# Optimization experiments

Hardware: AMD Instinct MI355X
Metric: run time of the kernel (lower is better)

## Reference

```python
import jax, jax.numpy as jnp
import numpy as np

B, S, D_IN, H = 4, 2048, 1024, 1024


def setup_inputs() -> dict:
    key = jax.random.key(0)
    k1, k2, k3 = jax.random.split(key, 3)
    qkv = jax.random.normal(k1, (B, S, D_IN), dtype=jnp.float32)
    # True = position is masked out (torch masked_fill semantics)
    attention_mask = jax.random.randint(k2, (B, S), 0, 2).astype(jnp.bool_)
    W_qkv = jax.random.normal(k3, (D_IN, 3 * H), dtype=jnp.float32) * (1.0 / np.sqrt(D_IN))
    b_qkv = jnp.zeros((3 * H,), dtype=jnp.float32)
    return {"qkv": qkv, "attention_mask": attention_mask, "W_qkv": W_qkv, "b_qkv": b_qkv}


def reference(qkv, attention_mask, W_qkv, b_qkv):
    # fused QKV projection: (B, S, 3H)
    proj = jnp.einsum("bsd,dh->bsh", qkv, W_qkv) + b_qkv
    q, k, v = jnp.split(proj, 3, axis=-1)  # each (B, S, H)
    scaling_factor = jnp.asarray(H, dtype=q.dtype) ** 0.5
    q = q * scaling_factor  # NOTE: original multiplies (not divides) by sqrt(H)
    scores = jnp.einsum("bqh,bkh->bqk", q, k)  # (B, S, S)
    # mask broadcasts over the query dim: masked keys get -inf
    neg_inf = jnp.asarray(-jnp.inf, dtype=scores.dtype)
    scores = jnp.where(attention_mask[:, None, :], neg_inf, scores)
    distributions = jax.nn.softmax(scores, axis=-1)  # dropout p=0.0 -> identity
    return jnp.einsum("bqk,bkh->bqh", distributions, v)
```

## Files before the change

kernel.cpp:

```cpp
#include <hip/hip_runtime.h>
#include <stdint.h>


#define S_LEN 2048
#define BATCH 4
#define DIN   1024
#define HDIM  1024
#define N3H   3072
#define NTOK  8192

typedef unsigned short u16;
typedef __attribute__((ext_vector_type(8))) short bf16x8;
typedef __attribute__((ext_vector_type(4))) float f32x4;
typedef __attribute__((ext_vector_type(16))) float f32x16;
typedef __attribute__((ext_vector_type(4))) unsigned short u16x4;

__device__ __forceinline__ u16 f2bf(float x) {
  union { float f; unsigned u; } c; c.f = x;
  unsigned r = c.u + 0x7fffu + ((c.u >> 16) & 1u);
  return (u16)(r >> 16);
}
__device__ __forceinline__ float bf2f(u16 h) {
  union { unsigned u; float f; } c; c.u = ((unsigned)h) << 16;
  return c.f;
}

__device__ __forceinline__ void gload16(const void* g, void* lds) {
  auto* gp = reinterpret_cast<const __attribute__((address_space(1))) void*>(
      reinterpret_cast<uintptr_t>(g));
  auto* lp = reinterpret_cast<__attribute__((address_space(3))) void*>(
      (unsigned)reinterpret_cast<uintptr_t>(lds));
  __builtin_amdgcn_global_load_lds(gp, lp, 16, 0, 0);
}

__device__ __forceinline__ void stage_tile(const u16* __restrict__ g, int ld,
                                           u16* lds, int wave, int lane) {
  const int rlane = lane >> 3;
  const int kb    = (lane & 7) ^ (rlane & 7);
#pragma unroll
  for (int h = 0; h < 4; ++h) {
    const int instr = wave * 4 + h;
    const u16* gp = g + (size_t)(instr * 8 + rlane) * ld + kb * 8;
    gload16(gp, (char*)lds + instr * 1024);
  }
}

__device__ __forceinline__ void stage_tile_idx(
    const u16* __restrict__ gbase, const int* __restrict__ idxb, int jbase,
    int k0, u16* lds, int wave, int lane) {
  const int rlane = lane >> 3;
  const int kb    = (lane & 7) ^ (rlane & 7);
#pragma unroll
  for (int h = 0; h < 4; ++h) {
    const int instr = wave * 4 + h;
    const int s = idxb[jbase + instr * 8 + rlane];
    const u16* gp = gbase + (size_t)s * DIN + k0 + kb * 8;
    gload16(gp, (char*)lds + instr * 1024);
  }
}

__device__ __forceinline__ bf16x8 frag32(const u16* t, int wq, int sub, int kh,
                                         int lane) {
  const int r5   = lane & 31;
  const int row  = wq * 64 + sub * 32 + r5;
  const int slot = (kh * 2 + (lane >> 5)) ^ (r5 & 7);
  return *(const bf16x8*)(t + row * 64 + slot * 8);
}

__device__ __forceinline__ void gemm_core_split(
    const u16* __restrict__ Ah, const u16* __restrict__ Al,
    const u16* __restrict__ Bh, const u16* __restrict__ Bl,
    int lda, int ldb, int K, f32x16 acc[2][2])
{
  __shared__ __align__(16) u16 lds[4 * 8192];
  u16* aH = lds;           u16* aL = lds + 8192;
  u16* bH = lds + 16384;   u16* bL = lds + 24576;
  const int tid  = threadIdx.x;
  const int wave = tid >> 6, lane = tid & 63;
  const int wm = wave >> 1, wn = wave & 1;

#pragma unroll
  for (int i = 0; i < 2; ++i)
#pragma unroll
    for (int j = 0; j < 2; ++j)
#pragma unroll
      for (int r = 0; r < 16; ++r) acc[i][j][r] = 0.f;

  for (int k0 = 0; k0 < K; k0 += 64) {
    stage_tile(Ah + k0, lda, aH, wave, lane);
    stage_tile(Al + k0, lda, aL, wave, lane);
    stage_tile(Bh + k0, ldb, bH, wave, lane);
    stage_tile(Bl + k0, ldb, bL, wave, lane);
    __syncthreads();

#pragma unroll
    for (int kh = 0; kh < 4; ++kh) {
      bf16x8 fah[2], fal[2];
#pragma unroll
      for (int i = 0; i < 2; ++i) {
        fah[i] = frag32(aH, wm, i, kh, lane);
        fal[i] = frag32(aL, wm, i, kh, lane);
      }
#pragma unroll
      for (int j = 0; j < 2; ++j) {
        const bf16x8 fbh = frag32(bH, wn, j, kh, lane);
        const bf16x8 fbl = frag32(bL, wn, j, kh, lane);
#pragma unroll
        for (int i = 0; i < 2; ++i) {
          acc[i][j] = __builtin_amdgcn_mfma_f32_32x32x16_bf16(fah[i], fbh, acc[i][j], 0, 0, 0);
          acc[i][j] = __builtin_amdgcn_mfma_f32_32x32x16_bf16(fah[i], fbl, acc[i][j], 0, 0, 0);
          acc[i][j] = __builtin_amdgcn_mfma_f32_32x32x16_bf16(fal[i], fbh, acc[i][j], 0, 0, 0);
        }
      }
    }
    __syncthreads();
  }
}

__device__ __forceinline__ void gemm_core_split_idx(
    const u16* __restrict__ Ah, const u16* __restrict__ Al,
    const int* __restrict__ idxb, int jbase,
    const u16* __restrict__ Bh, const u16* __restrict__ Bl,
    f32x16 acc[2][2])
{
  __shared__ __align__(16) u16 lds[4 * 8192];
  u16* aH = lds;           u16* aL = lds + 8192;
  u16* bH = lds + 16384;   u16* bL = lds + 24576;
  const int tid  = threadIdx.x;
  const int wave = tid >> 6, lane = tid & 63;
  const int wm = wave >> 1, wn = wave & 1;

#pragma unroll
  for (int i = 0; i < 2; ++i)
#pragma unroll
    for (int j = 0; j < 2; ++j)
#pragma unroll
      for (int r = 0; r < 16; ++r) acc[i][j][r] = 0.f;

  for (int k0 = 0; k0 < DIN; k0 += 64) {
    stage_tile_idx(Ah, idxb, jbase, k0, aH, wave, lane);
    stage_tile_idx(Al, idxb, jbase, k0, aL, wave, lane);
    stage_tile(Bh + k0, DIN, bH, wave, lane);
    stage_tile(Bl + k0, DIN, bL, wave, lane);
    __syncthreads();

#pragma unroll
    for (int kh = 0; kh < 4; ++kh) {
      bf16x8 fah[2], fal[2];
#pragma unroll
      for (int i = 0; i < 2; ++i) {
        fah[i] = frag32(aH, wm, i, kh, lane);
        fal[i] = frag32(aL, wm, i, kh, lane);
      }
#pragma unroll
      for (int j = 0; j < 2; ++j) {
        const bf16x8 fbh = frag32(bH, wn, j, kh, lane);
        const bf16x8 fbl = frag32(bL, wn, j, kh, lane);
#pragma unroll
        for (int i = 0; i < 2; ++i) {
          acc[i][j] = __builtin_amdgcn_mfma_f32_32x32x16_bf16(fah[i], fbh, acc[i][j], 0, 0, 0);
          acc[i][j] = __builtin_amdgcn_mfma_f32_32x32x16_bf16(fah[i], fbl, acc[i][j], 0, 0, 0);
          acc[i][j] = __builtin_amdgcn_mfma_f32_32x32x16_bf16(fal[i], fbh, acc[i][j], 0, 0, 0);
        }
      }
    }
    __syncthreads();
  }
}

__device__ __forceinline__ void gemm_core_plain(
    const u16* __restrict__ A, const u16* __restrict__ B,
    int lda, int ldb, int K, f32x16 acc[2][2])
{
  __shared__ __align__(16) u16 lds[2 * 8192];
  u16* aT = lds; u16* bT = lds + 8192;
  const int tid  = threadIdx.x;
  const int wave = tid >> 6, lane = tid & 63;
  const int wm = wave >> 1, wn = wave & 1;

#pragma unroll
  for (int i = 0; i < 2; ++i)
#pragma unroll
    for (int j = 0; j < 2; ++j)
#pragma unroll
      for (int r = 0; r < 16; ++r) acc[i][j][r] = 0.f;

  for (int k0 = 0; k0 < K; k0 += 64) {
    stage_tile(A + k0, lda, aT, wave, lane);
    stage_tile(B + k0, ldb, bT, wave, lane);
    __syncthreads();
#pragma unroll
    for (int kh = 0; kh < 4; ++kh) {
      bf16x8 fa[2];
#pragma unroll
      for (int i = 0; i < 2; ++i) fa[i] = frag32(aT, wm, i, kh, lane);
#pragma unroll
      for (int j = 0; j < 2; ++j) {
        const bf16x8 fb = frag32(bT, wn, j, kh, lane);
#pragma unroll
        for (int i = 0; i < 2; ++i)
          acc[i][j] = __builtin_amdgcn_mfma_f32_32x32x16_bf16(fa[i], fb, acc[i][j], 0, 0, 0);
      }
    }
    __syncthreads();
  }
}

__device__ __forceinline__ void gemm_core_plain_idx(
    const u16* __restrict__ A, const int* __restrict__ idxb, int jbase,
    const u16* __restrict__ B, f32x16 acc[2][2])
{
  __shared__ __align__(16) u16 lds[2 * 8192];
  u16* aT = lds; u16* bT = lds + 8192;
  const int tid  = threadIdx.x;
  const int wave = tid >> 6, lane = tid & 63;
  const int wm = wave >> 1, wn = wave & 1;

#pragma unroll
  for (int i = 0; i < 2; ++i)
#pragma unroll
    for (int j = 0; j < 2; ++j)
#pragma unroll
      for (int r = 0; r < 16; ++r) acc[i][j][r] = 0.f;

  for (int k0 = 0; k0 < DIN; k0 += 64) {
    stage_tile_idx(A, idxb, jbase, k0, aT, wave, lane);
    stage_tile(B + k0, DIN, bT, wave, lane);
    __syncthreads();
#pragma unroll
    for (int kh = 0; kh < 4; ++kh) {
      bf16x8 fa[2];
#pragma unroll
      for (int i = 0; i < 2; ++i) fa[i] = frag32(aT, wm, i, kh, lane);
#pragma unroll
      for (int j = 0; j < 2; ++j) {
        const bf16x8 fb = frag32(bT, wn, j, kh, lane);
#pragma unroll
        for (int i = 0; i < 2; ++i)
          acc[i][j] = __builtin_amdgcn_mfma_f32_32x32x16_bf16(fa[i], fb, acc[i][j], 0, 0, 0);
      }
    }
    __syncthreads();
  }
}

#define ROW32(r, lane) (((r) & 3) + 8 * ((r) >> 2) + 4 * ((lane) >> 5))

__global__ void prep_kernel(const unsigned char* __restrict__ m,
                            int* __restrict__ idx, int* __restrict__ kcount) {
  __shared__ int isBool;
  if (threadIdx.x == 0) isBool = 0;
  __syncthreads();
  for (int i = threadIdx.x; i < NTOK; i += 256)
    if ((i & 3) && m[i]) isBool = 1;
  __syncthreads();
  const int stride = isBool ? 1 : 4;
  const int wave = threadIdx.x >> 6, lane = threadIdx.x & 63;
  const int b = wave;
  const int base = b * S_LEN;
  int running = 0;
#pragma unroll 1
  for (int c = 0; c < S_LEN / 64; ++c) {
    const int s = c * 64 + lane;
    const int um = (m[(size_t)(base + s) * stride] == 0);
    const unsigned long long bal = __ballot(um);
    const int pre = (int)__popcll(bal & ((1ULL << lane) - 1ULL));
    if (um) idx[base + running + pre] = s;
    running += (int)__popcll(bal);
  }
  if (lane == 0) kcount[b] = running;
  for (int j = running + lane; j < S_LEN; j += 64) idx[base + j] = 0;
}

__global__ __launch_bounds__(256) void split_f32_kernel(
    const float* __restrict__ x, u16* __restrict__ hi, u16* __restrict__ lo) {
  const int i = (blockIdx.x * 256 + threadIdx.x) * 4;
  const f32x4 v = *(const f32x4*)(x + i);
  u16x4 h, l;
#pragma unroll
  for (int c = 0; c < 4; ++c) {
    h[c] = f2bf(v[c]);
    l[c] = f2bf(v[c] - bf2f(h[c]));
  }
  *(u16x4*)(hi + i) = h;
  *(u16x4*)(lo + i) = l;
}

__global__ __launch_bounds__(256) void splitWT_kernel(
    const float* __restrict__ W, u16* __restrict__ whi, u16* __restrict__ wlo) {
  __shared__ float tile[32][33];
  const int t = threadIdx.x;
  const int n0 = blockIdx.x * 32;
  const int d0 = blockIdx.y * 32;
  const int dr = t >> 3, nc = (t & 7) * 4;
  const f32x4 v = *(const f32x4*)(W + (size_t)(d0 + dr) * N3H + n0 + nc);
#pragma unroll
  for (int c = 0; c < 4; ++c) tile[dr][nc + c] = v[c];
  __syncthreads();
  const int nr = t >> 3, dc = (t & 7) * 4;
  u16x4 h, l;
#pragma unroll
  for (int c = 0; c < 4; ++c) {
    const float x = tile[dc + c][nr];
    h[c] = f2bf(x);
    l[c] = f2bf(x - bf2f(h[c]));
  }
  const size_t o = (size_t)(n0 + nr) * DIN + d0 + dc;
  *(u16x4*)(whi + o) = h;
  *(u16x4*)(wlo + o) = l;
}

__global__ __launch_bounds__(256, 2) void proj_q_kernel(
    const u16* __restrict__ Ahi, const u16* __restrict__ Alo,
    const u16* __restrict__ Whi, const u16* __restrict__ Wlo,
    const float* __restrict__ bias,
    u16* __restrict__ qhi, u16* __restrict__ qlo)
{
  const int bx = blockIdx.x, by = blockIdx.y;
  f32x16 acc[2][2];
  gemm_core_split(Ahi + (size_t)by * 128 * DIN, Alo + (size_t)by * 128 * DIN,
                  Whi + (size_t)bx * 128 * DIN, Wlo + (size_t)bx * 128 * DIN,
                  DIN, DIN, DIN, acc);
  const int lane = threadIdx.x & 63, wave = threadIdx.x >> 6;
  const int wm = wave >> 1, wn = wave & 1;
#pragma unroll
  for (int i = 0; i < 2; ++i) {
#pragma unroll
    for (int j = 0; j < 2; ++j) {
#pragma unroll
      for (int r = 0; r < 16; ++r) {
        const int row = by * 128 + wm * 64 + i * 32 + ROW32(r, lane);
        const int col = bx * 128 + wn * 64 + j * 32 + (lane & 31);
        const float v = acc[i][j][r] + bias[col];
        const u16 h = f2bf(v);
        const u16 l = f2bf(v - bf2f(h));
        const size_t idx = (size_t)row * HDIM + col;
        qhi[idx] = h; qlo[idx] = l;
      }
    }
  }
}

__global__ __launch_bounds__(256, 2) void proj_k_kernel(
    const u16* __restrict__ Ahi, const u16* __restrict__ Alo,
    const u16* __restrict__ Whi, const u16* __restrict__ Wlo,
    const float* __restrict__ bias,
    const int* __restrict__ idx, const int* __restrict__ kcount,
    u16* __restrict__ khi, u16* __restrict__ klo)
{
  const int id = blockIdx.x;
  const int t  = id >> 5;
  const int rs = id & 31;
  const int b  = rs >> 3;
  const int bx = rs & 7;
  const int cnt = kcount[b];
  if (t * 128 >= cnt) return;

  f32x16 acc[2][2];
  gemm_core_split_idx(Ahi + (size_t)b * S_LEN * DIN, Alo + (size_t)b * S_LEN * DIN,
                      idx + b * S_LEN, t * 128,
                      Whi + (size_t)(HDIM + bx * 128) * DIN,
                      Wlo + (size_t)(HDIM + bx * 128) * DIN, acc);
  const int lane = threadIdx.x & 63, wave = threadIdx.x >> 6;
  const int wm = wave >> 1, wn = wave & 1;
#pragma unroll
  for (int i = 0; i < 2; ++i) {
#pragma unroll
    for (int j = 0; j < 2; ++j) {
#pragma unroll
      for (int r = 0; r < 16; ++r) {
        const int jl   = t * 128 + wm * 64 + i * 32 + ROW32(r, lane);
        const int hcol = bx * 128 + wn * 64 + j * 32 + (lane & 31);
        const float v = acc[i][j][r] + bias[HDIM + hcol];
        const u16 h = f2bf(v);
        const u16 l = f2bf(v - bf2f(h));
        const size_t o = ((size_t)b * S_LEN + jl) * HDIM + hcol;
        khi[o] = h; klo[o] = l;
      }
    }
  }
}

__global__ __launch_bounds__(256, 2) void proj_v_kernel(
    const u16* __restrict__ Ahi, const u16* __restrict__ Whi,
    const float* __restrict__ bias,
    const int* __restrict__ idx, const int* __restrict__ kcount,
    u16* __restrict__ vt)
{
  const int id = blockIdx.x;
  const int t  = id >> 5;
  const int rs = id & 31;
  const int b  = rs >> 3;
  const int bx = rs & 7;
  const int cnt = kcount[b];
  if (t * 128 >= cnt) return;

  f32x16 acc[2][2];
  gemm_core_plain_idx(Ahi + (size_t)b * S_LEN * DIN, idx + b * S_LEN, t * 128,
                      Whi + (size_t)(2048 + bx * 128) * DIN, acc);
  const int lane = threadIdx.x & 63, wave = threadIdx.x >> 6;
  const int wm = wave >> 1, wn = wave & 1;
#pragma unroll
  for (int i = 0; i < 2; ++i) {
#pragma unroll
    for (int j = 0; j < 2; ++j) {
#pragma unroll
      for (int r = 0; r < 16; ++r) {
        const int jl   = t * 128 + wm * 64 + i * 32 + ROW32(r, lane);
        const int hcol = bx * 128 + wn * 64 + j * 32 + (lane & 31);
        const float v = acc[i][j][r] + bias[2 * HDIM + hcol];
        vt[((size_t)b * HDIM + hcol) * S_LEN + jl] = f2bf(v);
      }
    }
  }
}

__global__ __launch_bounds__(256, 2) void scores_kernel(
    const u16* __restrict__ qhi, const u16* __restrict__ qlo,
    const u16* __restrict__ khi, const u16* __restrict__ klo,
    const int* __restrict__ kcount, float* __restrict__ scores)
{
  const int id = blockIdx.x;
  const int bx = id >> 6;
  const int b  = (id >> 4) & 3;
  const int by = id & 15;
  const int cnt = kcount[b];
  if (bx * 128 >= cnt) return;

  f32x16 acc[2][2];
  const size_t qoff = ((size_t)b * S_LEN + by * 128) * HDIM;
  const size_t koff = ((size_t)b * S_LEN + bx * 128) * HDIM;
  gemm_core_split(qhi + qoff, qlo + qoff, khi + koff, klo + koff,
                  HDIM, HDIM, HDIM, acc);
  const int lane = threadIdx.x & 63, wave = threadIdx.x >> 6;
  const int wm = wave >> 1, wn = wave & 1;
#pragma unroll
  for (int i = 0; i < 2; ++i) {
#pragma unroll
    for (int j = 0; j < 2; ++j) {
#pragma unroll
      for (int rr = 0; rr < 16; ++rr) {
        const int q   = by * 128 + wm * 64 + i * 32 + ROW32(rr, lane);
        const int key = bx * 128 + wn * 64 + j * 32 + (lane & 31);
        scores[((size_t)b * S_LEN + q) * S_LEN + key] = 32.0f * acc[i][j][rr];
      }
    }
  }
}

__global__ __launch_bounds__(256) void softmax_kernel(
    float* __restrict__ scores, const int* __restrict__ kcount) {
  const int wave = threadIdx.x >> 6, lane = threadIdx.x & 63;
  const int row = blockIdx.x * 4 + wave;
  const int b = row >> 11;
  const int cnt = kcount[b];
  const int nc = (cnt + 255) >> 8;
  float* srow = scores + (size_t)row * S_LEN;
  const float ninf = -__builtin_inff();

  f32x4 v[8];
  float m = ninf;
#pragma unroll
  for (int c = 0; c < 8; ++c) {
    if (c < nc) {
      v[c] = ((const f32x4*)srow)[c * 64 + lane];
      const int j0 = c * 256 + lane * 4;
#pragma unroll
      for (int e = 0; e < 4; ++e) {
        if (j0 + e >= cnt) v[c][e] = ninf;
        m = fmaxf(m, v[c][e]);
      }
    }
  }
#pragma unroll
  for (int o = 32; o > 0; o >>= 1) m = fmaxf(m, __shfl_xor(m, o));

  float s = 0.f;
#pragma unroll
  for (int c = 0; c < 8; ++c) {
    if (c < nc) {
#pragma unroll
      for (int e = 0; e < 4; ++e) {
        v[c][e] = __expf(v[c][e] - m);
        s += v[c][e];
      }
    }
  }
#pragma unroll
  for (int o = 32; o > 0; o >>= 1) s += __shfl_xor(s, o);
  const float inv = 1.0f / s;

  u16* prow = (u16*)srow;
#pragma unroll
  for (int c = 0; c < 8; ++c) {
    if (c < nc) {
      u16x4 o4 = { f2bf(v[c][0] * inv), f2bf(v[c][1] * inv),
                   f2bf(v[c][2] * inv), f2bf(v[c][3] * inv) };
      ((u16x4*)prow)[c * 64 + lane] = o4;
    }
  }
}

__global__ __launch_bounds__(256, 2) void pv_kernel(
    const u16* __restrict__ P, const u16* __restrict__ vt,
    const int* __restrict__ kcount, float* __restrict__ out)
{
  const int id   = blockIdx.x;
  const int xcd  = id & 7;
  const int s    = id >> 3;
  const int b    = s >> 4;
  const int slot = s & 15;
  const int bx   = (xcd & 1) * 4 + (slot & 3);
  const int by   = (xcd >> 1) * 4 + (slot >> 2);
  const int cnt  = kcount[b];
  const int K    = (cnt + 63) & ~63;

  f32x16 acc[2][2];
  gemm_core_plain(P + ((size_t)b * S_LEN + by * 128) * (2 * S_LEN),
                  vt + ((size_t)b * HDIM + bx * 128) * S_LEN,
                  2 * S_LEN, S_LEN, K, acc);
  const int lane = threadIdx.x & 63, wave = threadIdx.x >> 6;
  const int wm = wave >> 1, wn = wave & 1;
#pragma unroll
  for (int i = 0; i < 2; ++i) {
#pragma unroll
    for (int j = 0; j < 2; ++j) {
#pragma unroll
      for (int r = 0; r < 16; ++r) {
        const int q = by * 128 + wm * 64 + i * 32 + ROW32(r, lane);
        const int h = bx * 128 + wn * 64 + j * 32 + (lane & 31);
        out[((size_t)b * S_LEN + q) * HDIM + h] = acc[i][j][r];
      }
    }
  }
}

extern "C" void kernel_launch(void* const* d_in, const int* in_sizes, int n_in,
                              void* d_out, int out_size, void* d_ws, size_t ws_size,
                              hipStream_t stream)
{
  const float* qkv  = (const float*)d_in[0];
  const void*  mask = d_in[1];
  const float* W    = (const float*)d_in[2];
  const float* bias = (const float*)d_in[3];
  float* out = (float*)d_out;
  char* ws = (char*)d_ws;

  const size_t off_cnt  = 0;
  const size_t off_idx  = 256;
  const size_t off_Whi  = 33024;
  const size_t off_Wlo  = off_Whi + (size_t)N3H * DIN * 2;
  const size_t off_Qhi  = off_Wlo + (size_t)N3H * DIN * 2;
  const size_t off_Qlo  = off_Qhi + (size_t)NTOK * HDIM * 2;
  const size_t off_Khi  = off_Qlo + (size_t)NTOK * HDIM * 2;
  const size_t off_Klo  = off_Khi + (size_t)NTOK * HDIM * 2;
  const size_t off_Vt   = off_Klo + (size_t)NTOK * HDIM * 2;
  const size_t off_A    = off_Vt + (size_t)NTOK * HDIM * 2;
  const size_t off_Alo  = off_A + (size_t)NTOK * DIN * 2;
  const size_t off_sc   = off_A;

  int* kcount = (int*)(ws + off_cnt);
  int* idx    = (int*)(ws + off_idx);
  u16* Whi = (u16*)(ws + off_Whi);  u16* Wlo = (u16*)(ws + off_Wlo);
  u16* Qhi = (u16*)(ws + off_Qhi);  u16* Qlo = (u16*)(ws + off_Qlo);
  u16* Khi = (u16*)(ws + off_Khi);  u16* Klo = (u16*)(ws + off_Klo);
  u16* Vt  = (u16*)(ws + off_Vt);
  u16* Ahi = (u16*)(ws + off_A);    u16* Alo = (u16*)(ws + off_Alo);
  float* scores = (float*)(ws + off_sc);

  prep_kernel<<<1, 256, 0, stream>>>((const unsigned char*)mask, idx, kcount);
  split_f32_kernel<<<NTOK * DIN / 1024, 256, 0, stream>>>(qkv, Ahi, Alo);
  splitWT_kernel<<<dim3(N3H / 32, DIN / 32), 256, 0, stream>>>(W, Whi, Wlo);
  proj_q_kernel<<<dim3(HDIM / 128, NTOK / 128), 256, 0, stream>>>(
      Ahi, Alo, Whi, Wlo, bias, Qhi, Qlo);
  proj_k_kernel<<<512, 256, 0, stream>>>(
      Ahi, Alo, Whi, Wlo, bias, idx, kcount, Khi, Klo);
  proj_v_kernel<<<512, 256, 0, stream>>>(
      Ahi, Whi, bias, idx, kcount, Vt);
  scores_kernel<<<16 * 16 * BATCH, 256, 0, stream>>>(
      Qhi, Qlo, Khi, Klo, kcount, scores);
  softmax_kernel<<<NTOK / 4, 256, 0, stream>>>(scores, kcount);
  pv_kernel<<<8 * 16 * BATCH, 256, 0, stream>>>(
      (const u16*)scores, Vt, kcount, out);
}
```

Measured before the change: 370.7 us.

## Fuse prep kernels, reorder scores grid, raise occupancy bounds for plain GEMMs

Merges the mask-compaction, input split and weight transpose-split kernels into one front kernel, removing two launches. Moves LDS buffers from the GEMM helpers into the kernels that call them. Raises the minimum-blocks launch bound from 2 to 4 for the V projection and PV kernels. Remaps scores block indices so the always-valid first eight key tiles come first and the mask-dependent tiles come after, giving a denser set of live blocks. These change scheduling and register pressure, and may cause spills in the kernels with the tighter bounds.

```diff
diff --git a/kernel.cpp b/kernel.cpp
--- a/kernel.cpp
+++ b/kernel.cpp
@@ -68,11 +68,11 @@
 }
 
 __device__ __forceinline__ void gemm_core_split(
+    u16* lds,
     const u16* __restrict__ Ah, const u16* __restrict__ Al,
     const u16* __restrict__ Bh, const u16* __restrict__ Bl,
     int lda, int ldb, int K, f32x16 acc[2][2])
 {
-  __shared__ __align__(16) u16 lds[4 * 8192];
   u16* aH = lds;           u16* aL = lds + 8192;
   u16* bH = lds + 16384;   u16* bL = lds + 24576;
   const int tid  = threadIdx.x;
@@ -118,12 +118,12 @@
 }
 
 __device__ __forceinline__ void gemm_core_split_idx(
+    u16* lds,
     const u16* __restrict__ Ah, const u16* __restrict__ Al,
     const int* __restrict__ idxb, int jbase,
     const u16* __restrict__ Bh, const u16* __restrict__ Bl,
     f32x16 acc[2][2])
 {
-  __shared__ __align__(16) u16 lds[4 * 8192];
   u16* aH = lds;           u16* aL = lds + 8192;
   u16* bH = lds + 16384;   u16* bL = lds + 24576;
   const int tid  = threadIdx.x;
@@ -169,10 +169,10 @@
 }
 
 __device__ __forceinline__ void gemm_core_plain(
+    u16* lds,
     const u16* __restrict__ A, const u16* __restrict__ B,
     int lda, int ldb, int K, f32x16 acc[2][2])
 {
-  __shared__ __align__(16) u16 lds[2 * 8192];
   u16* aT = lds; u16* bT = lds + 8192;
   const int tid  = threadIdx.x;
   const int wave = tid >> 6, lane = tid & 63;
@@ -207,10 +207,10 @@
 }
 
 __device__ __forceinline__ void gemm_core_plain_idx(
+    u16* lds,
     const u16* __restrict__ A, const int* __restrict__ idxb, int jbase,
     const u16* __restrict__ B, f32x16 acc[2][2])
 {
-  __shared__ __align__(16) u16 lds[2 * 8192];
   u16* aT = lds; u16* bT = lds + 8192;
   const int tid  = threadIdx.x;
   const int wave = tid >> 6, lane = tid & 63;
@@ -246,68 +246,72 @@
 
 #define ROW32(r, lane) (((r) & 3) + 8 * ((r) >> 2) + 4 * ((lane) >> 5))
 
-__global__ void prep_kernel(const unsigned char* __restrict__ m,
-                            int* __restrict__ idx, int* __restrict__ kcount) {
+__global__ __launch_bounds__(256) void front_kernel(
+    const float* __restrict__ qkv, const float* __restrict__ W,
+    const unsigned char* __restrict__ m,
+    u16* __restrict__ ahi, u16* __restrict__ alo,
+    u16* __restrict__ whi, u16* __restrict__ wlo,
+    int* __restrict__ idx, int* __restrict__ kcount)
+{
+  __shared__ float tile[32][33];
   __shared__ int isBool;
-  if (threadIdx.x == 0) isBool = 0;
-  __syncthreads();
-  for (int i = threadIdx.x; i < NTOK; i += 256)
-    if ((i & 3) && m[i]) isBool = 1;
-  __syncthreads();
-  const int stride = isBool ? 1 : 4;
-  const int wave = threadIdx.x >> 6, lane = threadIdx.x & 63;
-  const int b = wave;
-  const int base = b * S_LEN;
-  int running = 0;
+  const int id = blockIdx.x;
+  const int t = threadIdx.x;
+
+  if (id < 8192) {
+    const int i = (id * 256 + t) * 4;
+    const f32x4 v = *(const f32x4*)(qkv + i);
+    u16x4 h, l;
+#pragma unroll
+    for (int c = 0; c < 4; ++c) {
+      h[c] = f2bf(v[c]);
+      l[c] = f2bf(v[c] - bf2f(h[c]));
+    }
+    *(u16x4*)(ahi + i) = h;
+    *(u16x4*)(alo + i) = l;
+  } else if (id < 11264) {
+    const int wid = id - 8192;
+    const int n0 = (wid % 96) * 32;
+    const int d0 = (wid / 96) * 32;
+    const int dr = t >> 3, nc = (t & 7) * 4;
+    const f32x4 v = *(const f32x4*)(W + (size_t)(d0 + dr) * N3H + n0 + nc);
+#pragma unroll
+    for (int c = 0; c < 4; ++c) tile[dr][nc + c] = v[c];
+    __syncthreads();
+    const int nr = t >> 3, dc = (t & 7) * 4;
+    u16x4 h, l;
+#pragma unroll
+    for (int c = 0; c < 4; ++c) {
+      const float x = tile[dc + c][nr];
+      h[c] = f2bf(x);
+      l[c] = f2bf(x - bf2f(h[c]));
+    }
+    const size_t o = (size_t)(n0 + nr) * DIN + d0 + dc;
+    *(u16x4*)(whi + o) = h;
+    *(u16x4*)(wlo + o) = l;
+  } else {
+    if (t == 0) isBool = 0;
+    __syncthreads();
+    for (int i = t; i < NTOK; i += 256)
+      if ((i & 3) && m[i]) isBool = 1;
+    __syncthreads();
+    const int stride = isBool ? 1 : 4;
+    const int wave = t >> 6, lane = t & 63;
+    const int b = wave;
+    const int base = b * S_LEN;
+    int running = 0;
 #pragma unroll 1
-  for (int c = 0; c < S_LEN / 64; ++c) {
-    const int s = c * 64 + lane;
-    const int um = (m[(size_t)(base + s) * stride] == 0);
-    const unsigned long long bal = __ballot(um);
-    const int pre = (int)__popcll(bal & ((1ULL << lane) - 1ULL));
-    if (um) idx[base + running + pre] = s;
-    running += (int)__popcll(bal);
-  }
-  if (lane == 0) kcount[b] = running;
-  for (int j = running + lane; j < S_LEN; j += 64) idx[base + j] = 0;
-}
-
-__global__ __launch_bounds__(256) void split_f32_kernel(
-    const float* __restrict__ x, u16* __restrict__ hi, u16* __restrict__ lo) {
-  const int i = (blockIdx.x * 256 + threadIdx.x) * 4;
-  const f32x4 v = *(const f32x4*)(x + i);
-  u16x4 h, l;
-#pragma unroll
-  for (int c = 0; c < 4; ++c) {
-    h[c] = f2bf(v[c]);
-    l[c] = f2bf(v[c] - bf2f(h[c]));
-  }
-  *(u16x4*)(hi + i) = h;
-  *(u16x4*)(lo + i) = l;
-}
-
-__global__ __launch_bounds__(256) void splitWT_kernel(
-    const float* __restrict__ W, u16* __restrict__ whi, u16* __restrict__ wlo) {
-  __shared__ float tile[32][33];
-  const int t = threadIdx.x;
-  const int n0 = blockIdx.x * 32;
-  const int d0 = blockIdx.y * 32;
-  const int dr = t >> 3, nc = (t & 7) * 4;
-  const f32x4 v = *(const f32x4*)(W + (size_t)(d0 + dr) * N3H + n0 + nc);
-#pragma unroll
-  for (int c = 0; c < 4; ++c) tile[dr][nc + c] = v[c];
-  __syncthreads();
-  const int nr = t >> 3, dc = (t & 7) * 4;
-  u16x4 h, l;
-#pragma unroll
-  for (int c = 0; c < 4; ++c) {
-    const float x = tile[dc + c][nr];
-    h[c] = f2bf(x);
-    l[c] = f2bf(x - bf2f(h[c]));
-  }
-  const size_t o = (size_t)(n0 + nr) * DIN + d0 + dc;
-  *(u16x4*)(whi + o) = h;
-  *(u16x4*)(wlo + o) = l;
+    for (int c = 0; c < S_LEN / 64; ++c) {
+      const int s = c * 64 + lane;
+      const int um = (m[(size_t)(base + s) * stride] == 0);
+      const unsigned long long bal = __ballot(um);
+      const int pre = (int)__popcll(bal & ((1ULL << lane) - 1ULL));
+      if (um) idx[base + running + pre] = s;
+      running += (int)__popcll(bal);
+    }
+    if (lane == 0) kcount[b] = running;
+    for (int j = running + lane; j < S_LEN; j += 64) idx[base + j] = 0;
+  }
 }
 
 __global__ __launch_bounds__(256, 2) void proj_q_kernel(
@@ -316,9 +320,11 @@
     const float* __restrict__ bias,
     u16* __restrict__ qhi, u16* __restrict__ qlo)
 {
+  __shared__ __align__(16) u16 lds[4 * 8192];
   const int bx = blockIdx.x, by = blockIdx.y;
   f32x16 acc[2][2];
-  gemm_core_split(Ahi + (size_t)by * 128 * DIN, Alo + (size_t)by * 128 * DIN,
+  gemm_core_split(lds,
+                  Ahi + (size_t)by * 128 * DIN, Alo + (size_t)by * 128 * DIN,
                   Whi + (size_t)bx * 128 * DIN, Wlo + (size_t)bx * 128 * DIN,
                   DIN, DIN, DIN, acc);
   const int lane = threadIdx.x & 63, wave = threadIdx.x >> 6;
@@ -334,8 +340,8 @@
         const float v = acc[i][j][r] + bias[col];
         const u16 h = f2bf(v);
         const u16 l = f2bf(v - bf2f(h));
-        const size_t idx = (size_t)row * HDIM + col;
-        qhi[idx] = h; qlo[idx] = l;
+        const size_t o = (size_t)row * HDIM + col;
+        qhi[o] = h; qlo[o] = l;
       }
     }
   }
@@ -348,6 +354,7 @@
     const int* __restrict__ idx, const int* __restrict__ kcount,
     u16* __restrict__ khi, u16* __restrict__ klo)
 {
+  __shared__ __align__(16) u16 lds[4 * 8192];
   const int id = blockIdx.x;
   const int t  = id >> 5;
   const int rs = id & 31;
@@ -357,7 +364,8 @@
   if (t * 128 >= cnt) return;
 
   f32x16 acc[2][2];
-  gemm_core_split_idx(Ahi + (size_t)b * S_LEN * DIN, Alo + (size_t)b * S_LEN * DIN,
+  gemm_core_split_idx(lds,
+                      Ahi + (size_t)b * S_LEN * DIN, Alo + (size_t)b * S_LEN * DIN,
                       idx + b * S_LEN, t * 128,
                       Whi + (size_t)(HDIM + bx * 128) * DIN,
                       Wlo + (size_t)(HDIM + bx * 128) * DIN, acc);
@@ -381,12 +389,13 @@
   }
 }
 
-__global__ __launch_bounds__(256, 2) void proj_v_kernel(
+__global__ __launch_bounds__(256, 4) void proj_v_kernel(
     const u16* __restrict__ Ahi, const u16* __restrict__ Whi,
     const float* __restrict__ bias,
     const int* __restrict__ idx, const int* __restrict__ kcount,
     u16* __restrict__ vt)
 {
+  __shared__ __align__(16) u16 lds[2 * 8192];
   const int id = blockIdx.x;
   const int t  = id >> 5;
   const int rs = id & 31;
@@ -396,7 +405,8 @@
   if (t * 128 >= cnt) return;
 
   f32x16 acc[2][2];
-  gemm_core_plain_idx(Ahi + (size_t)b * S_LEN * DIN, idx + b * S_LEN, t * 128,
+  gemm_core_plain_idx(lds,
+                      Ahi + (size_t)b * S_LEN * DIN, idx + b * S_LEN, t * 128,
                       Whi + (size_t)(2048 + bx * 128) * DIN, acc);
   const int lane = threadIdx.x & 63, wave = threadIdx.x >> 6;
   const int wm = wave >> 1, wn = wave & 1;
@@ -420,17 +430,18 @@
     const u16* __restrict__ khi, const u16* __restrict__ klo,
     const int* __restrict__ kcount, float* __restrict__ scores)
 {
+  __shared__ __align__(16) u16 lds[4 * 8192];
   const int id = blockIdx.x;
-  const int bx = id >> 6;
-  const int b  = (id >> 4) & 3;
-  const int by = id & 15;
+  int b, by, bx;
+  if (id < 512) { bx = id & 7; const int r = id >> 3; b = r >> 4; by = r & 15; }
+  else { const int w = id - 512; bx = 8 + (w >> 6); const int r = w & 63; b = r >> 4; by = r & 15; }
   const int cnt = kcount[b];
   if (bx * 128 >= cnt) return;
 
   f32x16 acc[2][2];
   const size_t qoff = ((size_t)b * S_LEN + by * 128) * HDIM;
   const size_t koff = ((size_t)b * S_LEN + bx * 128) * HDIM;
-  gemm_core_split(qhi + qoff, qlo + qoff, khi + koff, klo + koff,
+  gemm_core_split(lds, qhi + qoff, qlo + qoff, khi + koff, klo + koff,
                   HDIM, HDIM, HDIM, acc);
   const int lane = threadIdx.x & 63, wave = threadIdx.x >> 6;
   const int wm = wave >> 1, wn = wave & 1;
@@ -501,10 +512,11 @@
   }
 }
 
-__global__ __launch_bounds__(256, 2) void pv_kernel(
+__global__ __launch_bounds__(256, 4) void pv_kernel(
     const u16* __restrict__ P, const u16* __restrict__ vt,
     const int* __restrict__ kcount, float* __restrict__ out)
 {
+  __shared__ __align__(16) u16 lds[2 * 8192];
   const int id   = blockIdx.x;
   const int xcd  = id & 7;
   const int s    = id >> 3;
@@ -516,7 +528,8 @@
   const int K    = (cnt + 63) & ~63;
 
   f32x16 acc[2][2];
-  gemm_core_plain(P + ((size_t)b * S_LEN + by * 128) * (2 * S_LEN),
+  gemm_core_plain(lds,
+                  P + ((size_t)b * S_LEN + by * 128) * (2 * S_LEN),
                   vt + ((size_t)b * HDIM + bx * 128) * S_LEN,
                   2 * S_LEN, S_LEN, K, acc);
   const int lane = threadIdx.x & 63, wave = threadIdx.x >> 6;
@@ -568,16 +581,15 @@
   u16* Ahi = (u16*)(ws + off_A);    u16* Alo = (u16*)(ws + off_Alo);
   float* scores = (float*)(ws + off_sc);
 
-  prep_kernel<<<1, 256, 0, stream>>>((const unsigned char*)mask, idx, kcount);
-  split_f32_kernel<<<NTOK * DIN / 1024, 256, 0, stream>>>(qkv, Ahi, Alo);
-  splitWT_kernel<<<dim3(N3H / 32, DIN / 32), 256, 0, stream>>>(W, Whi, Wlo);
+  front_kernel<<<11265, 256, 0, stream>>>(
+      qkv, W, (const unsigned char*)mask, Ahi, Alo, Whi, Wlo, idx, kcount);
   proj_q_kernel<<<dim3(HDIM / 128, NTOK / 128), 256, 0, stream>>>(
       Ahi, Alo, Whi, Wlo, bias, Qhi, Qlo);
   proj_k_kernel<<<512, 256, 0, stream>>>(
       Ahi, Alo, Whi, Wlo, bias, idx, kcount, Khi, Klo);
   proj_v_kernel<<<512, 256, 0, stream>>>(
       Ahi, Whi, bias, idx, kcount, Vt);
-  scores_kernel<<<16 * 16 * BATCH, 256, 0, stream>>>(
+  scores_kernel<<<1024, 256, 0, stream>>>(
       Qhi, Qlo, Khi, Klo, kcount, scores);
   softmax_kernel<<<NTOK / 4, 256, 0, stream>>>(scores, kcount);
   pv_kernel<<<8 * 16 * BATCH, 256, 0, stream>>>(
```

Measured after the change: 383.5 us. 1.03x slower.
